# Kernel tuning notes

Hardware: AMD Instinct MI355X
Metric: run time of the kernel (lower is better)

Reference implementation:

```python
import jax, jax.numpy as jnp
import numpy as np

D_MODEL = 512
H = 8
D_K = D_MODEL // H


def setup_inputs() -> dict:
    key = jax.random.key(0)
    ks = jax.random.split(key, 11)
    B, S = 2, 4096
    scale = 1.0 / np.sqrt(D_MODEL)
    inp = {
        "q": jax.random.normal(ks[0], (B, S, D_MODEL), jnp.float32),
        "k": jax.random.normal(ks[1], (B, S, D_MODEL), jnp.float32),
        "v": jax.random.normal(ks[2], (B, S, D_MODEL), jnp.float32),
        "wq": jax.random.normal(ks[3], (D_MODEL, D_MODEL), jnp.float32) * scale,
        "bq": jnp.zeros((D_MODEL,), jnp.float32),
        "wk": jax.random.normal(ks[4], (D_MODEL, D_MODEL), jnp.float32) * scale,
        "bk": jnp.zeros((D_MODEL,), jnp.float32),
        "wv": jax.random.normal(ks[5], (D_MODEL, D_MODEL), jnp.float32) * scale,
        "bv": jnp.zeros((D_MODEL,), jnp.float32),
        "wo": jax.random.normal(ks[6], (D_MODEL, D_MODEL), jnp.float32) * scale,
        "bo": jnp.zeros((D_MODEL,), jnp.float32),
    }
    return inp


def reference(q, k, v, wq, bq, wk, bk, wv, bv, wo, bo):
    B, S, _ = q.shape
    # Linear projections (torch Linear: x @ W.T + b), split into heads -> [B,H,S,Dk]
    def proj(x, w, b):
        y = jnp.einsum('bsd,ed->bse', x, w) + b
        return y.reshape(B, -1, H, D_K).transpose(0, 2, 1, 3)

    qh = proj(q, wq, bq)
    kh = proj(k, wk, bk)
    vh = proj(v, wv, bv)

    # scaled dot-product attention, full [B,H,S,S] scores (faithful to source)
    scores = jnp.einsum('bhqd,bhkd->bhqk', qh, kh) / jnp.sqrt(jnp.asarray(D_K, qh.dtype))
    attn = jax.nn.softmax(scores, axis=-1)
    x = jnp.einsum('bhqk,bhkd->bhqd', attn, vh)

    # merge heads and output projection
    x = x.transpose(0, 2, 1, 3).reshape(B, S, H * D_K)
    return jnp.einsum('bsd,ed->bse', x, wo) + bo
```

## Files before the change

kernel.cpp:

```cpp
#include <hip/hip_runtime.h>

#define DM 512
#define NH 8
#define DK 64
#define SEQ 4096

typedef short bf16x8 __attribute__((ext_vector_type(8)));
typedef float f32x4 __attribute__((ext_vector_type(4)));
typedef unsigned short u16;
typedef u16 u16x8 __attribute__((ext_vector_type(8)));
typedef u16 u16x4 __attribute__((ext_vector_type(4)));
typedef unsigned int u32;
typedef u32 u32x2 __attribute__((ext_vector_type(2)));

__device__ __forceinline__ u16 f2bf(float f) {
  union { float f; unsigned u; } v; v.f = f;
  unsigned r = v.u + 0x7fffu + ((v.u >> 16) & 1u);
  return (u16)(r >> 16);
}

__device__ __forceinline__ u32 cvtpk(float a, float b) {
  u32 r; asm("v_cvt_pk_bf16_f32 %0, %1, %2" : "=v"(r) : "v"(a), "v"(b)); return r;
}

__device__ __forceinline__ float fexp2(float x) {
  float r; asm("v_exp_f32 %0, %1" : "=v"(r) : "v"(x)); return r;
}

__device__ __forceinline__ float fmax3(float a, float b, float c) {
  return fmaxf(fmaxf(a, b), c);
}

__global__ __launch_bounds__(256, 2)
void gemm_qkv(const float* __restrict__ qx, const float* __restrict__ kx,
              const float* __restrict__ vx,
              const float* __restrict__ wq, const float* __restrict__ bq,
              const float* __restrict__ wk, const float* __restrict__ bk,
              const float* __restrict__ wv, const float* __restrict__ bv,
              u16* __restrict__ Qh, u16* __restrict__ Kh, u16* __restrict__ Vt)
{
  __shared__ alignas(16) u16 Alds[64][72];
  __shared__ alignas(16) u16 Blds[128][72];
  const int mode = blockIdx.x >> 9;
  const int bid = blockIdx.x & 511;
  const float* X = (mode == 0) ? qx : (mode == 1) ? kx : vx;
  const float* W = (mode == 0) ? wq : (mode == 1) ? wk : wv;
  const float* Bs = (mode == 0) ? bq : (mode == 1) ? bk : bv;

  const int t = threadIdx.x;
  const int bx = bid & 127, by = bid >> 7;
  const int m0 = bx << 6, n0 = by << 7;
  const int lane = t & 63, w = t >> 6;
  const int lr = lane & 15, lg = lane >> 4;
  const int wr = w >> 1, wc = w & 1;

  f32x4 acc[2][4];
  #pragma unroll
  for (int i = 0; i < 2; ++i)
    #pragma unroll
    for (int j = 0; j < 4; ++j) acc[i][j] = (f32x4){0.f, 0.f, 0.f, 0.f};

  float4 xa[4]; float4 wb[8];
  auto loadX = [&](int k0) {
    #pragma unroll
    for (int i = 0; i < 4; ++i) {
      int f = (i << 8) + t;
      xa[i] = *(const float4*)(X + (size_t)(m0 + (f >> 4)) * 512 + k0 + ((f & 15) << 2));
    }
    #pragma unroll
    for (int i = 0; i < 8; ++i) {
      int f = (i << 8) + t;
      wb[i] = *(const float4*)(W + (size_t)(n0 + (f >> 4)) * 512 + k0 + ((f & 15) << 2));
    }
  };

  loadX(0);
  for (int k0 = 0; k0 < 512; k0 += 64) {
    __syncthreads();
    #pragma unroll
    for (int i = 0; i < 4; ++i) {
      int f = (i << 8) + t;
      u16x4 p = { f2bf(xa[i].x), f2bf(xa[i].y), f2bf(xa[i].z), f2bf(xa[i].w) };
      *(u16x4*)&Alds[f >> 4][(f & 15) << 2] = p;
    }
    #pragma unroll
    for (int i = 0; i < 8; ++i) {
      int f = (i << 8) + t;
      u16x4 p = { f2bf(wb[i].x), f2bf(wb[i].y), f2bf(wb[i].z), f2bf(wb[i].w) };
      *(u16x4*)&Blds[f >> 4][(f & 15) << 2] = p;
    }
    __syncthreads();
    if (k0 + 64 < 512) loadX(k0 + 64);

    #pragma unroll
    for (int kk = 0; kk < 2; ++kk) {
      bf16x8 af[2], bfr[4];
      #pragma unroll
      for (int mi = 0; mi < 2; ++mi)
        af[mi] = *(const bf16x8*)&Alds[(wr << 5) + (mi << 4) + lr][(kk << 5) + (lg << 3)];
      #pragma unroll
      for (int ni = 0; ni < 4; ++ni)
        bfr[ni] = *(const bf16x8*)&Blds[(wc << 6) + (ni << 4) + lr][(kk << 5) + (lg << 3)];
      #pragma unroll
      for (int mi = 0; mi < 2; ++mi)
        #pragma unroll
        for (int ni = 0; ni < 4; ++ni)
          acc[mi][ni] = __builtin_amdgcn_mfma_f32_16x16x32_bf16(af[mi], bfr[ni], acc[mi][ni], 0, 0, 0);
    }
  }

  const float sc = (mode == 0) ? 0.18033688f : 1.0f;
  #pragma unroll
  for (int mi = 0; mi < 2; ++mi) {
    #pragma unroll
    for (int ni = 0; ni < 4; ++ni) {
      const int e = n0 + (wc << 6) + (ni << 4) + lr;
      const int m = m0 + (wr << 5) + (mi << 4) + (lg << 2);
      const float bb = Bs[e];
      const int b = m >> 12, s = m & 4095, h = e >> 6, dk = e & 63;
      if (mode != 2) {
        u16* O = (mode == 0) ? Qh : Kh;
        size_t base = ((size_t)((b << 3) + h) * SEQ + s) * DK + dk;
        #pragma unroll
        for (int r = 0; r < 4; ++r)
          O[base + (size_t)r * DK] = f2bf((acc[mi][ni][r] + bb) * sc);
      } else {
        size_t base = ((size_t)((b << 3) + h) * DK + dk) * SEQ + s;
        u16x4 p = { f2bf(acc[mi][ni][0] + bb), f2bf(acc[mi][ni][1] + bb),
                    f2bf(acc[mi][ni][2] + bb), f2bf(acc[mi][ni][3] + bb) };
        *(u16x4*)(Vt + base) = p;
      }
    }
  }
}

__global__ __launch_bounds__(256, 2)
void gemm_out(const u16* __restrict__ Xa, const float* __restrict__ W,
              const float* __restrict__ bias, float* __restrict__ Out)
{
  __shared__ alignas(16) u16 Alds[64][72];
  __shared__ alignas(16) u16 Blds[128][72];
  const int t = threadIdx.x;
  const int bx = blockIdx.x & 127, by = blockIdx.x >> 7;
  const int m0 = bx << 6, n0 = by << 7;
  const int lane = t & 63, w = t >> 6;
  const int lr = lane & 15, lg = lane >> 4;
  const int wr = w >> 1, wc = w & 1;

  f32x4 acc[2][4];
  #pragma unroll
  for (int i = 0; i < 2; ++i)
    #pragma unroll
    for (int j = 0; j < 4; ++j) acc[i][j] = (f32x4){0.f, 0.f, 0.f, 0.f};

  u16x8 xa3[2]; float4 wb[8];
  auto loadX = [&](int k0) {
    #pragma unroll
    for (int i = 0; i < 2; ++i) {
      int f = (i << 8) + t;
      xa3[i] = *(const u16x8*)(Xa + (size_t)(m0 + (f >> 3)) * 512 + k0 + ((f & 7) << 3));
    }
    #pragma unroll
    for (int i = 0; i < 8; ++i) {
      int f = (i << 8) + t;
      wb[i] = *(const float4*)(W + (size_t)(n0 + (f >> 4)) * 512 + k0 + ((f & 15) << 2));
    }
  };

  loadX(0);
  for (int k0 = 0; k0 < 512; k0 += 64) {
    __syncthreads();
    #pragma unroll
    for (int i = 0; i < 2; ++i) {
      int f = (i << 8) + t;
      *(u16x8*)&Alds[f >> 3][(f & 7) << 3] = xa3[i];
    }
    #pragma unroll
    for (int i = 0; i < 8; ++i) {
      int f = (i << 8) + t;
      u16x4 p = { f2bf(wb[i].x), f2bf(wb[i].y), f2bf(wb[i].z), f2bf(wb[i].w) };
      *(u16x4*)&Blds[f >> 4][(f & 15) << 2] = p;
    }
    __syncthreads();
    if (k0 + 64 < 512) loadX(k0 + 64);

    #pragma unroll
    for (int kk = 0; kk < 2; ++kk) {
      bf16x8 af[2], bfr[4];
      #pragma unroll
      for (int mi = 0; mi < 2; ++mi)
        af[mi] = *(const bf16x8*)&Alds[(wr << 5) + (mi << 4) + lr][(kk << 5) + (lg << 3)];
      #pragma unroll
      for (int ni = 0; ni < 4; ++ni)
        bfr[ni] = *(const bf16x8*)&Blds[(wc << 6) + (ni << 4) + lr][(kk << 5) + (lg << 3)];
      #pragma unroll
      for (int mi = 0; mi < 2; ++mi)
        #pragma unroll
        for (int ni = 0; ni < 4; ++ni)
          acc[mi][ni] = __builtin_amdgcn_mfma_f32_16x16x32_bf16(af[mi], bfr[ni], acc[mi][ni], 0, 0, 0);
    }
  }

  #pragma unroll
  for (int mi = 0; mi < 2; ++mi) {
    #pragma unroll
    for (int ni = 0; ni < 4; ++ni) {
      const int e = n0 + (wc << 6) + (ni << 4) + lr;
      const int m = m0 + (wr << 5) + (mi << 4) + (lg << 2);
      const float bb = bias[e];
      size_t base = (size_t)m * 512 + e;
      #pragma unroll
      for (int r = 0; r < 4; ++r) Out[base + (size_t)r * 512] = acc[mi][ni][r] + bb;
    }
  }
}

__global__ __launch_bounds__(256, 2)
void attn_kernel(const u16* __restrict__ Qh, const u16* __restrict__ Kh,
                 const u16* __restrict__ Vt, u16* __restrict__ Xa)
{
  __shared__ alignas(1024) u16 smem[20992];

  const int t = threadIdx.x;
  const int lane = t & 63, w = t >> 6;
  const int lr = lane & 15, lg = lane >> 4;
  const int ob = ((blockIdx.x & 7) << 6) + (blockIdx.x >> 3);
  const int qb = ob & 31, bh = ob >> 5;
  const size_t qkbase = (size_t)bh * SEQ * DK;
  const size_t vbase  = (size_t)bh * DK * SEQ;
  u16* Pw = smem + 16384 + w * 1152;

  bf16x8 qf[2][2];
  #pragma unroll
  for (int mi = 0; mi < 2; ++mi)
    #pragma unroll
    for (int kk = 0; kk < 2; ++kk) {
      int qrow = (qb << 7) + (w << 5) + (mi << 4) + lr;
      qf[mi][kk] = *(const bf16x8*)(Qh + qkbase + (size_t)qrow * DK + (kk << 5) + (lg << 3));
    }

  bf16x8 onesf;
  {
    u16 one = (lr == 0) ? (u16)0x3F80 : (u16)0;
    #pragma unroll
    for (int j = 0; j < 8; ++j) onesf[j] = (short)one;
  }

  float mrun[2] = {-3e38f, -3e38f};
  f32x4 o[2][4], osum[2];
  #pragma unroll
  for (int mi = 0; mi < 2; ++mi) {
    #pragma unroll
    for (int dt = 0; dt < 4; ++dt) o[mi][dt] = (f32x4){0.f, 0.f, 0.f, 0.f};
    osum[mi] = (f32x4){0.f, 0.f, 0.f, 0.f};
  }

  const u16* Kg = Kh + qkbase;
  const u16* Vg = Vt + vbase;
  const int r0 = t >> 3, c0 = t & 7;
  const int r1 = r0 + 32;
  const int wk0 = r0 * 64 + ((c0 ^ (r0 & 7)) << 3);
  const int wk1 = r1 * 64 + ((c0 ^ (r1 & 7)) << 3);

  u16x8 kr0, kr1, vr0, vr1;
  auto GLOAD = [&](int it2) {
    const int kv0 = it2 << 6;
    kr0 = *(const u16x8*)(Kg + (size_t)(kv0 + r0) * 64 + (c0 << 3));
    kr1 = *(const u16x8*)(Kg + (size_t)(kv0 + r1) * 64 + (c0 << 3));
    vr0 = *(const u16x8*)(Vg + (size_t)r0 * SEQ + kv0 + (c0 << 3));
    vr1 = *(const u16x8*)(Vg + (size_t)r1 * SEQ + kv0 + (c0 << 3));
  };
  auto WRITE = [&](int buf) {
    u16* B = smem + buf * 8192;
    *(u16x8*)&B[wk0]        = kr0;
    *(u16x8*)&B[wk1]        = kr1;
    *(u16x8*)&B[4096 + wk0] = vr0;
    *(u16x8*)&B[4096 + wk1] = vr1;
  };

  GLOAD(0); WRITE(0); GLOAD(1);

  for (int it = 0; it < SEQ / 64; ++it) {
    const int cur = it & 1;
    __syncthreads();

    const u16* Kb = smem + cur * 8192;
    const u16* Vb = Kb + 4096;
    bf16x8 kf[4][2], vf[4][2];
    #pragma unroll
    for (int nt = 0; nt < 4; ++nt)
      #pragma unroll
      for (int kk = 0; kk < 2; ++kk) {
        const int off = ((nt << 4) + lr) * 64 + ((((kk << 2) + lg) ^ (lr & 7)) << 3);
        kf[nt][kk] = *(const bf16x8*)&Kb[off];
        vf[nt][kk] = *(const bf16x8*)&Vb[off];
      }

    if (it + 1 < SEQ / 64) WRITE(cur ^ 1);
    if (it + 2 < SEQ / 64) GLOAD(it + 2);

    #pragma unroll
    for (int mi = 0; mi < 2; ++mi) {
      f32x4 s[4];
      #pragma unroll
      for (int nt = 0; nt < 4; ++nt) s[nt] = (f32x4){0.f, 0.f, 0.f, 0.f};
      #pragma unroll
      for (int kk = 0; kk < 2; ++kk)
        #pragma unroll
        for (int nt = 0; nt < 4; ++nt)
          s[nt] = __builtin_amdgcn_mfma_f32_16x16x32_bf16(kf[nt][kk], qf[mi][kk], s[nt], 0, 0, 0);

      float m0 = fmax3(s[0][0], s[0][1], s[0][2]);
      float m1 = fmax3(s[0][3], s[1][0], s[1][1]);
      float m2 = fmax3(s[1][2], s[1][3], s[2][0]);
      float m3 = fmax3(s[2][1], s[2][2], s[2][3]);
      float m4 = fmax3(s[3][0], s[3][1], s[3][2]);
      float tmax = fmaxf(fmax3(m0, m1, m2), fmax3(m3, m4, s[3][3]));
      tmax = fmaxf(tmax, __shfl_xor(tmax, 16));
      tmax = fmaxf(tmax, __shfl_xor(tmax, 32));

      if (!__all(tmax <= mrun[mi] + 8.f)) {
        float mnew = fmaxf(mrun[mi], tmax);
        float scl = fexp2(mrun[mi] - mnew);
        mrun[mi] = mnew;
        osum[mi][0] *= scl;
        #pragma unroll
        for (int dt = 0; dt < 4; ++dt) o[mi][dt] *= scl;
      }
      const float mm = mrun[mi];

      #pragma unroll
      for (int nt = 0; nt < 4; ++nt) {
        float e0 = fexp2(s[nt][0] - mm), e1 = fexp2(s[nt][1] - mm);
        float e2 = fexp2(s[nt][2] - mm), e3 = fexp2(s[nt][3] - mm);
        u32x2 pk2 = { cvtpk(e0, e1), cvtpk(e2, e3) };
        *(u32x2*)((char*)Pw + lr * 144 + (nt << 5) + (lg << 3)) = pk2;
      }

      #pragma unroll
      for (int kk = 0; kk < 2; ++kk) {
        bf16x8 pf = *(const bf16x8*)&Pw[lr * 72 + (kk << 5) + (lg << 3)];
        #pragma unroll
        for (int dt = 0; dt < 4; ++dt)
          o[mi][dt] = __builtin_amdgcn_mfma_f32_16x16x32_bf16(vf[dt][kk], pf, o[mi][dt], 0, 0, 0);
        osum[mi] = __builtin_amdgcn_mfma_f32_16x16x32_bf16(onesf, pf, osum[mi], 0, 0, 0);
      }
    }
  }
  __syncthreads();

  #pragma unroll
  for (int mi = 0; mi < 2; ++mi) {
    float lsum = __shfl(osum[mi][0], lr);
    float inv = 1.f / lsum;
    #pragma unroll
    for (int dt = 0; dt < 4; ++dt) {
      u16x4 v4 = { f2bf(o[mi][dt][0] * inv), f2bf(o[mi][dt][1] * inv),
                   f2bf(o[mi][dt][2] * inv), f2bf(o[mi][dt][3] * inv) };
      int row = (w << 5) + (mi << 4) + lr;
      *(u16x4*)&smem[row * 72 + (dt << 4) + (lg << 2)] = v4;
    }
  }
  __syncthreads();
  {
    const int b = bh >> 3, h = bh & 7;
    #pragma unroll
    for (int i = 0; i < 4; ++i) {
      int f = (i << 8) + t;
      int row = f >> 3, c8 = (f & 7) << 3;
      u16x8 val = *(const u16x8*)&smem[row * 72 + c8];
      *(u16x8*)(Xa + ((size_t)b * SEQ + (qb << 7) + row) * DM + (h << 6) + c8) = val;
    }
  }
}

extern "C" void kernel_launch(void* const* d_in, const int* in_sizes, int n_in,
                              void* d_out, int out_size, void* d_ws, size_t ws_size,
                              hipStream_t stream)
{
  const float* q  = (const float*)d_in[0];
  const float* k  = (const float*)d_in[1];
  const float* v  = (const float*)d_in[2];
  const float* wq = (const float*)d_in[3];
  const float* bq = (const float*)d_in[4];
  const float* wk = (const float*)d_in[5];
  const float* bk = (const float*)d_in[6];
  const float* wv = (const float*)d_in[7];
  const float* bv = (const float*)d_in[8];
  const float* wo = (const float*)d_in[9];
  const float* bo = (const float*)d_in[10];

  const size_t HS = (size_t)2 * NH * SEQ * DK;
  u16* Qh = (u16*)d_ws;
  u16* Kh = Qh + HS;
  u16* Vt = Kh + HS;
  u16* Xa = Vt + HS;

  gemm_qkv<<<1536, 256, 0, stream>>>(q, k, v, wq, bq, wk, bk, wv, bv, Qh, Kh, Vt);
  attn_kernel<<<512, 256, 0, stream>>>(Qh, Kh, Vt, Xa);
  gemm_out<<<512, 256, 0, stream>>>(Xa, wo, bo, (float*)d_out);
}
```

Baseline: 146.1 us.

## Double-buffer LDS in projection GEMMs and defer softmax max shuffles

Both projection GEMM kernels now use two LDS buffers, so each K-step needs one barrier instead of two. The next tile is converted and written into the other buffer after the MFMAs, while the global load for the tile after that is issued. In the attention kernel, the cross-lane shuffles for the row max run only when a lane's partial max exceeds the running max by the threshold, which removes two shuffles from the common path. The cost is double the LDS per block for the GEMMs, which may lower occupancy.

```diff
diff --git a/kernel.cpp b/kernel.cpp
--- a/kernel.cpp
+++ b/kernel.cpp
@@ -39,8 +39,8 @@
               const float* __restrict__ wv, const float* __restrict__ bv,
               u16* __restrict__ Qh, u16* __restrict__ Kh, u16* __restrict__ Vt)
 {
-  __shared__ alignas(16) u16 Alds[64][72];
-  __shared__ alignas(16) u16 Blds[128][72];
+  __shared__ alignas(16) u16 Alds[2][64][72];
+  __shared__ alignas(16) u16 Blds[2][128][72];
   const int mode = blockIdx.x >> 9;
   const int bid = blockIdx.x & 511;
   const float* X = (mode == 0) ? qx : (mode == 1) ? kx : vx;
@@ -73,40 +73,43 @@
       wb[i] = *(const float4*)(W + (size_t)(n0 + (f >> 4)) * 512 + k0 + ((f & 15) << 2));
     }
   };
-
-  loadX(0);
-  for (int k0 = 0; k0 < 512; k0 += 64) {
+  auto WRITE = [&](int buf) {
+    #pragma unroll
+    for (int i = 0; i < 4; ++i) {
+      int f = (i << 8) + t;
+      u16x4 p = { f2bf(xa[i].x), f2bf(xa[i].y), f2bf(xa[i].z), f2bf(xa[i].w) };
+      *(u16x4*)&Alds[buf][f >> 4][(f & 15) << 2] = p;
+    }
+    #pragma unroll
+    for (int i = 0; i < 8; ++i) {
+      int f = (i << 8) + t;
+      u16x4 p = { f2bf(wb[i].x), f2bf(wb[i].y), f2bf(wb[i].z), f2bf(wb[i].w) };
+      *(u16x4*)&Blds[buf][f >> 4][(f & 15) << 2] = p;
+    }
+  };
+
+  loadX(0); WRITE(0); loadX(64);
+  for (int it = 0; it < 8; ++it) {
+    const int cur = it & 1;
     __syncthreads();
-    #pragma unroll
-    for (int i = 0; i < 4; ++i) {
-      int f = (i << 8) + t;
-      u16x4 p = { f2bf(xa[i].x), f2bf(xa[i].y), f2bf(xa[i].z), f2bf(xa[i].w) };
-      *(u16x4*)&Alds[f >> 4][(f & 15) << 2] = p;
-    }
-    #pragma unroll
-    for (int i = 0; i < 8; ++i) {
-      int f = (i << 8) + t;
-      u16x4 p = { f2bf(wb[i].x), f2bf(wb[i].y), f2bf(wb[i].z), f2bf(wb[i].w) };
-      *(u16x4*)&Blds[f >> 4][(f & 15) << 2] = p;
-    }
-    __syncthreads();
-    if (k0 + 64 < 512) loadX(k0 + 64);
 
     #pragma unroll
     for (int kk = 0; kk < 2; ++kk) {
       bf16x8 af[2], bfr[4];
       #pragma unroll
       for (int mi = 0; mi < 2; ++mi)
-        af[mi] = *(const bf16x8*)&Alds[(wr << 5) + (mi << 4) + lr][(kk << 5) + (lg << 3)];
+        af[mi] = *(const bf16x8*)&Alds[cur][(wr << 5) + (mi << 4) + lr][(kk << 5) + (lg << 3)];
       #pragma unroll
       for (int ni = 0; ni < 4; ++ni)
-        bfr[ni] = *(const bf16x8*)&Blds[(wc << 6) + (ni << 4) + lr][(kk << 5) + (lg << 3)];
+        bfr[ni] = *(const bf16x8*)&Blds[cur][(wc << 6) + (ni << 4) + lr][(kk << 5) + (lg << 3)];
       #pragma unroll
       for (int mi = 0; mi < 2; ++mi)
         #pragma unroll
         for (int ni = 0; ni < 4; ++ni)
           acc[mi][ni] = __builtin_amdgcn_mfma_f32_16x16x32_bf16(af[mi], bfr[ni], acc[mi][ni], 0, 0, 0);
     }
+    if (it + 1 < 8) WRITE(cur ^ 1);
+    if (it + 2 < 8) loadX((it + 2) << 6);
   }
 
   const float sc = (mode == 0) ? 0.18033688f : 1.0f;
@@ -138,8 +141,8 @@
 void gemm_out(const u16* __restrict__ Xa, const float* __restrict__ W,
               const float* __restrict__ bias, float* __restrict__ Out)
 {
-  __shared__ alignas(16) u16 Alds[64][72];
-  __shared__ alignas(16) u16 Blds[128][72];
+  __shared__ alignas(16) u16 Alds[2][64][72];
+  __shared__ alignas(16) u16 Blds[2][128][72];
   const int t = threadIdx.x;
   const int bx = blockIdx.x & 127, by = blockIdx.x >> 7;
   const int m0 = bx << 6, n0 = by << 7;
@@ -166,39 +169,42 @@
       wb[i] = *(const float4*)(W + (size_t)(n0 + (f >> 4)) * 512 + k0 + ((f & 15) << 2));
     }
   };
-
-  loadX(0);
-  for (int k0 = 0; k0 < 512; k0 += 64) {
+  auto WRITE = [&](int buf) {
+    #pragma unroll
+    for (int i = 0; i < 2; ++i) {
+      int f = (i << 8) + t;
+      *(u16x8*)&Alds[buf][f >> 3][(f & 7) << 3] = xa3[i];
+    }
+    #pragma unroll
+    for (int i = 0; i < 8; ++i) {
+      int f = (i << 8) + t;
+      u16x4 p = { f2bf(wb[i].x), f2bf(wb[i].y), f2bf(wb[i].z), f2bf(wb[i].w) };
+      *(u16x4*)&Blds[buf][f >> 4][(f & 15) << 2] = p;
+    }
+  };
+
+  loadX(0); WRITE(0); loadX(64);
+  for (int it = 0; it < 8; ++it) {
+    const int cur = it & 1;
     __syncthreads();
-    #pragma unroll
-    for (int i = 0; i < 2; ++i) {
-      int f = (i << 8) + t;
-      *(u16x8*)&Alds[f >> 3][(f & 7) << 3] = xa3[i];
-    }
-    #pragma unroll
-    for (int i = 0; i < 8; ++i) {
-      int f = (i << 8) + t;
-      u16x4 p = { f2bf(wb[i].x), f2bf(wb[i].y), f2bf(wb[i].z), f2bf(wb[i].w) };
-      *(u16x4*)&Blds[f >> 4][(f & 15) << 2] = p;
-    }
-    __syncthreads();
-    if (k0 + 64 < 512) loadX(k0 + 64);
 
     #pragma unroll
     for (int kk = 0; kk < 2; ++kk) {
       bf16x8 af[2], bfr[4];
       #pragma unroll
       for (int mi = 0; mi < 2; ++mi)
-        af[mi] = *(const bf16x8*)&Alds[(wr << 5) + (mi << 4) + lr][(kk << 5) + (lg << 3)];
+        af[mi] = *(const bf16x8*)&Alds[cur][(wr << 5) + (mi << 4) + lr][(kk << 5) + (lg << 3)];
       #pragma unroll
       for (int ni = 0; ni < 4; ++ni)
-        bfr[ni] = *(const bf16x8*)&Blds[(wc << 6) + (ni << 4) + lr][(kk << 5) + (lg << 3)];
+        bfr[ni] = *(const bf16x8*)&Blds[cur][(wc << 6) + (ni << 4) + lr][(kk << 5) + (lg << 3)];
       #pragma unroll
       for (int mi = 0; mi < 2; ++mi)
         #pragma unroll
         for (int ni = 0; ni < 4; ++ni)
           acc[mi][ni] = __builtin_amdgcn_mfma_f32_16x16x32_bf16(af[mi], bfr[ni], acc[mi][ni], 0, 0, 0);
     }
+    if (it + 1 < 8) WRITE(cur ^ 1);
+    if (it + 2 < 8) loadX((it + 2) << 6);
   }
 
   #pragma unroll
@@ -315,11 +321,11 @@
       float m2 = fmax3(s[1][2], s[1][3], s[2][0]);
       float m3 = fmax3(s[2][1], s[2][2], s[2][3]);
       float m4 = fmax3(s[3][0], s[3][1], s[3][2]);
-      float tmax = fmaxf(fmax3(m0, m1, m2), fmax3(m3, m4, s[3][3]));
-      tmax = fmaxf(tmax, __shfl_xor(tmax, 16));
-      tmax = fmaxf(tmax, __shfl_xor(tmax, 32));
-
-      if (!__all(tmax <= mrun[mi] + 8.f)) {
+      float pmax = fmaxf(fmax3(m0, m1, m2), fmax3(m3, m4, s[3][3]));
+
+      if (!__all(pmax <= mrun[mi] + 8.f)) {
+        float tmax = fmaxf(pmax, __shfl_xor(pmax, 16));
+        tmax = fmaxf(tmax, __shfl_xor(tmax, 32));
         float mnew = fmaxf(mrun[mi], tmax);
         float scl = fexp2(mrun[mi] - mnew);
         mrun[mi] = mnew;
```

Result: faster. 141.9 us (-2.9%).

## Enlarge GEMM tiles to 128x128, remap blocks per XCD, defer softmax max shuffles

Applied to the files above, without the earlier changes.

Both projection GEMMs move from 64x128 to 128x128 output tiles, which halves the grid and doubles per-wave accumulators, so each loaded weight tile is reused across more rows. Blocks are remapped so that consecutive M tiles land on the same XCD, which should improve L2 locality. In attention, the cross-lane max reduction is moved inside the rare rescale branch and the threshold test uses the per-lane partial max. The larger tiles raise register and LDS use and leave fewer blocks to fill the CUs.

```diff
diff --git a/kernel.cpp b/kernel.cpp
--- a/kernel.cpp
+++ b/kernel.cpp
@@ -39,37 +39,35 @@
               const float* __restrict__ wv, const float* __restrict__ bv,
               u16* __restrict__ Qh, u16* __restrict__ Kh, u16* __restrict__ Vt)
 {
-  __shared__ alignas(16) u16 Alds[64][72];
+  __shared__ alignas(16) u16 Alds[128][72];
   __shared__ alignas(16) u16 Blds[128][72];
-  const int mode = blockIdx.x >> 9;
-  const int bid = blockIdx.x & 511;
+  const int mode = blockIdx.x >> 8;
+  const int d = blockIdx.x & 255;
+  const int xcd = d & 7, inner = d >> 3;
+  const int bx = (xcd << 3) + (inner >> 2);
+  const int by = inner & 3;
   const float* X = (mode == 0) ? qx : (mode == 1) ? kx : vx;
   const float* W = (mode == 0) ? wq : (mode == 1) ? wk : wv;
   const float* Bs = (mode == 0) ? bq : (mode == 1) ? bk : bv;
 
   const int t = threadIdx.x;
-  const int bx = bid & 127, by = bid >> 7;
-  const int m0 = bx << 6, n0 = by << 7;
+  const int m0 = bx << 7, n0 = by << 7;
   const int lane = t & 63, w = t >> 6;
   const int lr = lane & 15, lg = lane >> 4;
   const int wr = w >> 1, wc = w & 1;
 
-  f32x4 acc[2][4];
-  #pragma unroll
-  for (int i = 0; i < 2; ++i)
+  f32x4 acc[4][4];
+  #pragma unroll
+  for (int i = 0; i < 4; ++i)
     #pragma unroll
     for (int j = 0; j < 4; ++j) acc[i][j] = (f32x4){0.f, 0.f, 0.f, 0.f};
 
-  float4 xa[4]; float4 wb[8];
+  float4 xa[8], wb[8];
   auto loadX = [&](int k0) {
     #pragma unroll
-    for (int i = 0; i < 4; ++i) {
+    for (int i = 0; i < 8; ++i) {
       int f = (i << 8) + t;
       xa[i] = *(const float4*)(X + (size_t)(m0 + (f >> 4)) * 512 + k0 + ((f & 15) << 2));
-    }
-    #pragma unroll
-    for (int i = 0; i < 8; ++i) {
-      int f = (i << 8) + t;
       wb[i] = *(const float4*)(W + (size_t)(n0 + (f >> 4)) * 512 + k0 + ((f & 15) << 2));
     }
   };
@@ -78,31 +76,27 @@
   for (int k0 = 0; k0 < 512; k0 += 64) {
     __syncthreads();
     #pragma unroll
-    for (int i = 0; i < 4; ++i) {
-      int f = (i << 8) + t;
-      u16x4 p = { f2bf(xa[i].x), f2bf(xa[i].y), f2bf(xa[i].z), f2bf(xa[i].w) };
-      *(u16x4*)&Alds[f >> 4][(f & 15) << 2] = p;
-    }
-    #pragma unroll
     for (int i = 0; i < 8; ++i) {
       int f = (i << 8) + t;
-      u16x4 p = { f2bf(wb[i].x), f2bf(wb[i].y), f2bf(wb[i].z), f2bf(wb[i].w) };
-      *(u16x4*)&Blds[f >> 4][(f & 15) << 2] = p;
+      u16x4 pa = { f2bf(xa[i].x), f2bf(xa[i].y), f2bf(xa[i].z), f2bf(xa[i].w) };
+      *(u16x4*)&Alds[f >> 4][(f & 15) << 2] = pa;
+      u16x4 pb = { f2bf(wb[i].x), f2bf(wb[i].y), f2bf(wb[i].z), f2bf(wb[i].w) };
+      *(u16x4*)&Blds[f >> 4][(f & 15) << 2] = pb;
     }
     __syncthreads();
     if (k0 + 64 < 512) loadX(k0 + 64);
 
     #pragma unroll
     for (int kk = 0; kk < 2; ++kk) {
-      bf16x8 af[2], bfr[4];
-      #pragma unroll
-      for (int mi = 0; mi < 2; ++mi)
-        af[mi] = *(const bf16x8*)&Alds[(wr << 5) + (mi << 4) + lr][(kk << 5) + (lg << 3)];
+      bf16x8 af[4], bfr[4];
+      #pragma unroll
+      for (int mi = 0; mi < 4; ++mi)
+        af[mi] = *(const bf16x8*)&Alds[(wr << 6) + (mi << 4) + lr][(kk << 5) + (lg << 3)];
       #pragma unroll
       for (int ni = 0; ni < 4; ++ni)
         bfr[ni] = *(const bf16x8*)&Blds[(wc << 6) + (ni << 4) + lr][(kk << 5) + (lg << 3)];
       #pragma unroll
-      for (int mi = 0; mi < 2; ++mi)
+      for (int mi = 0; mi < 4; ++mi)
         #pragma unroll
         for (int ni = 0; ni < 4; ++ni)
           acc[mi][ni] = __builtin_amdgcn_mfma_f32_16x16x32_bf16(af[mi], bfr[ni], acc[mi][ni], 0, 0, 0);
@@ -111,11 +105,11 @@
 
   const float sc = (mode == 0) ? 0.18033688f : 1.0f;
   #pragma unroll
-  for (int mi = 0; mi < 2; ++mi) {
+  for (int mi = 0; mi < 4; ++mi) {
     #pragma unroll
     for (int ni = 0; ni < 4; ++ni) {
       const int e = n0 + (wc << 6) + (ni << 4) + lr;
-      const int m = m0 + (wr << 5) + (mi << 4) + (lg << 2);
+      const int m = m0 + (wr << 6) + (mi << 4) + (lg << 2);
       const float bb = Bs[e];
       const int b = m >> 12, s = m & 4095, h = e >> 6, dk = e & 63;
       if (mode != 2) {
@@ -138,25 +132,29 @@
 void gemm_out(const u16* __restrict__ Xa, const float* __restrict__ W,
               const float* __restrict__ bias, float* __restrict__ Out)
 {
-  __shared__ alignas(16) u16 Alds[64][72];
+  __shared__ alignas(16) u16 Alds[128][72];
   __shared__ alignas(16) u16 Blds[128][72];
+  const int d = blockIdx.x;
+  const int xcd = d & 7, inner = d >> 3;
+  const int bx = (xcd << 3) + (inner >> 2);
+  const int by = inner & 3;
+
   const int t = threadIdx.x;
-  const int bx = blockIdx.x & 127, by = blockIdx.x >> 7;
-  const int m0 = bx << 6, n0 = by << 7;
+  const int m0 = bx << 7, n0 = by << 7;
   const int lane = t & 63, w = t >> 6;
   const int lr = lane & 15, lg = lane >> 4;
   const int wr = w >> 1, wc = w & 1;
 
-  f32x4 acc[2][4];
-  #pragma unroll
-  for (int i = 0; i < 2; ++i)
+  f32x4 acc[4][4];
+  #pragma unroll
+  for (int i = 0; i < 4; ++i)
     #pragma unroll
     for (int j = 0; j < 4; ++j) acc[i][j] = (f32x4){0.f, 0.f, 0.f, 0.f};
 
-  u16x8 xa3[2]; float4 wb[8];
+  u16x8 xa3[4]; float4 wb[8];
   auto loadX = [&](int k0) {
     #pragma unroll
-    for (int i = 0; i < 2; ++i) {
+    for (int i = 0; i < 4; ++i) {
       int f = (i << 8) + t;
       xa3[i] = *(const u16x8*)(Xa + (size_t)(m0 + (f >> 3)) * 512 + k0 + ((f & 7) << 3));
     }
@@ -171,7 +169,7 @@
   for (int k0 = 0; k0 < 512; k0 += 64) {
     __syncthreads();
     #pragma unroll
-    for (int i = 0; i < 2; ++i) {
+    for (int i = 0; i < 4; ++i) {
       int f = (i << 8) + t;
       *(u16x8*)&Alds[f >> 3][(f & 7) << 3] = xa3[i];
     }
@@ -186,15 +184,15 @@
 
     #pragma unroll
     for (int kk = 0; kk < 2; ++kk) {
-      bf16x8 af[2], bfr[4];
-      #pragma unroll
-      for (int mi = 0; mi < 2; ++mi)
-        af[mi] = *(const bf16x8*)&Alds[(wr << 5) + (mi << 4) + lr][(kk << 5) + (lg << 3)];
+      bf16x8 af[4], bfr[4];
+      #pragma unroll
+      for (int mi = 0; mi < 4; ++mi)
+        af[mi] = *(const bf16x8*)&Alds[(wr << 6) + (mi << 4) + lr][(kk << 5) + (lg << 3)];
       #pragma unroll
       for (int ni = 0; ni < 4; ++ni)
         bfr[ni] = *(const bf16x8*)&Blds[(wc << 6) + (ni << 4) + lr][(kk << 5) + (lg << 3)];
       #pragma unroll
-      for (int mi = 0; mi < 2; ++mi)
+      for (int mi = 0; mi < 4; ++mi)
         #pragma unroll
         for (int ni = 0; ni < 4; ++ni)
           acc[mi][ni] = __builtin_amdgcn_mfma_f32_16x16x32_bf16(af[mi], bfr[ni], acc[mi][ni], 0, 0, 0);
@@ -202,11 +200,11 @@
   }
 
   #pragma unroll
-  for (int mi = 0; mi < 2; ++mi) {
+  for (int mi = 0; mi < 4; ++mi) {
     #pragma unroll
     for (int ni = 0; ni < 4; ++ni) {
       const int e = n0 + (wc << 6) + (ni << 4) + lr;
-      const int m = m0 + (wr << 5) + (mi << 4) + (lg << 2);
+      const int m = m0 + (wr << 6) + (mi << 4) + (lg << 2);
       const float bb = bias[e];
       size_t base = (size_t)m * 512 + e;
       #pragma unroll
@@ -315,11 +313,11 @@
       float m2 = fmax3(s[1][2], s[1][3], s[2][0]);
       float m3 = fmax3(s[2][1], s[2][2], s[2][3]);
       float m4 = fmax3(s[3][0], s[3][1], s[3][2]);
-      float tmax = fmaxf(fmax3(m0, m1, m2), fmax3(m3, m4, s[3][3]));
-      tmax = fmaxf(tmax, __shfl_xor(tmax, 16));
-      tmax = fmaxf(tmax, __shfl_xor(tmax, 32));
-
-      if (!__all(tmax <= mrun[mi] + 8.f)) {
+      float pmax = fmaxf(fmax3(m0, m1, m2), fmax3(m3, m4, s[3][3]));
+
+      if (!__all(pmax <= mrun[mi] + 8.f)) {
+        float tmax = fmaxf(pmax, __shfl_xor(pmax, 16));
+        tmax = fmaxf(tmax, __shfl_xor(tmax, 32));
         float mnew = fmaxf(mrun[mi], tmax);
         float scl = fexp2(mrun[mi] - mnew);
         mrun[mi] = mnew;
@@ -396,7 +394,7 @@
   u16* Vt = Kh + HS;
   u16* Xa = Vt + HS;
 
-  gemm_qkv<<<1536, 256, 0, stream>>>(q, k, v, wq, bq, wk, bk, wv, bv, Qh, Kh, Vt);
+  gemm_qkv<<<768, 256, 0, stream>>>(q, k, v, wq, bq, wk, bk, wv, bv, Qh, Kh, Vt);
   attn_kernel<<<512, 256, 0, stream>>>(Qh, Kh, Vt, Xa);
-  gemm_out<<<512, 256, 0, stream>>>(Xa, wo, bo, (float*)d_out);
-}
+  gemm_out<<<256, 256, 0, stream>>>(Xa, wo, bo, (float*)d_out);
+}
```

Measured after the change: 138.5 us. 1.06x faster.
